# Kernel optimization log

Measured on AMD Instinct MI355X. Metric: run time of the kernel, lower is better.

Reference implementation:

```python
import jax, jax.numpy as jnp
import numpy as np

C = 128         # sphere_channels
H = 512         # hidden_channels
EC = 128        # edge_channels
LMAX = 4
K = 4           # num_experts
N_EQ = 2        # ceil(K/2) equivariant experts
N_NE = 2
N_NODES = 8192
N_EDGES = 262144
DEG_SIZES = np.array([2 * l + 1 for l in range(LMAX + 1)])  # [1,3,5,7,9]
M = int(DEG_SIZES.sum())  # 25 coeffs


def setup_inputs() -> dict:
    key = jax.random.key(0)
    ks = jax.random.split(key, 20)
    s = 0.02
    return {
        "x_emb": jax.random.normal(ks[0], (N_NODES, M, C), jnp.float32),
        "t_ij": jax.random.normal(ks[1], (N_EDGES, EC), jnp.float32),
        "edge_index": jax.random.randint(ks[2], (2, N_EDGES), 0, N_NODES, jnp.int32),
        # equivariant experts (stacked on leading expert axis)
        "eq_w1": jax.random.normal(ks[3], (N_EQ, C, H), jnp.float32) * s,
        "eq_gate_w": jax.random.normal(ks[4], (N_EQ, EC, H * (LMAX + 1)), jnp.float32) * s,
        "eq_gate_b": jax.random.normal(ks[5], (N_EQ, H * (LMAX + 1)), jnp.float32) * s,
        "eq_w2": jax.random.normal(ks[6], (N_EQ, H, C), jnp.float32) * s,
        # non-equivariant experts
        "ne_w1": jax.random.normal(ks[7], (N_NE, C, H), jnp.float32) * s,
        "ne_b1": jax.random.normal(ks[8], (N_NE, H), jnp.float32) * s,
        "ne_gate_w": jax.random.normal(ks[9], (N_NE, EC, H), jnp.float32) * s,
        "ne_gate_b": jax.random.normal(ks[10], (N_NE, H), jnp.float32) * s,
        "ne_w2": jax.random.normal(ks[11], (N_NE, H, C), jnp.float32) * s,
        "ne_b2": jax.random.normal(ks[12], (N_NE, C), jnp.float32) * s,
        # router
        "r_w1": jax.random.normal(ks[13], (EC, EC), jnp.float32) * s,
        "r_b1": jax.random.normal(ks[14], (EC,), jnp.float32) * s,
        "r_w2": jax.random.normal(ks[15], (EC, K), jnp.float32) * s,
        "r_b2": jax.random.normal(ks[16], (K,), jnp.float32) * s,
    }


def reference(x_emb, t_ij, edge_index, eq_w1, eq_gate_w, eq_gate_b, eq_w2,
              ne_w1, ne_b1, ne_gate_w, ne_gate_b, ne_w2, ne_b2,
              r_w1, r_b1, r_w2, r_b2):
    N = x_emb.shape[0]
    silu = jax.nn.silu

    # c_i = scatter-mean of t_ij onto destination nodes
    dst = edge_index[1]
    sums = jax.ops.segment_sum(t_ij, dst, num_segments=N)
    cnt = jax.ops.segment_sum(jnp.ones((t_ij.shape[0],), t_ij.dtype), dst, num_segments=N)
    c = sums / jnp.maximum(cnt, 1.0)[:, None]  # [N, EC]

    # soft routing weights from context
    w = jax.nn.softmax(silu(c @ r_w1 + r_b1) @ r_w2 + r_b2, axis=-1)  # [N, K]

    repeats = jnp.asarray(DEG_SIZES)
    is_scalar = (jnp.arange(M) == 0)[:, None]  # l=0 coeff mask, [M,1]

    # --- equivariant experts (vectorized over expert axis e) ---
    h = jnp.einsum('nmc,ech->enmh', x_emb, eq_w1)                      # [e,N,M,H]
    g = silu(jnp.einsum('nc,ecg->eng', c, eq_gate_w) + eq_gate_b[:, None, :])
    g = g.reshape(N_EQ, N, LMAX + 1, H)
    g = jnp.repeat(g, repeats, axis=2, total_repeat_length=M)          # [e,N,M,H]
    h = jnp.where(is_scalar, silu(h), h) * g                           # SiLU only on l=0
    out_eq = jnp.einsum('enmh,ehc->enmc', h, eq_w2)

    # --- non-equivariant experts ---
    h2 = silu(jnp.einsum('nmc,ech->enmh', x_emb, ne_w1) + ne_b1[:, None, None, :])
    g2 = silu(jnp.einsum('nc,ech->enh', c, ne_gate_w) + ne_gate_b[:, None, :])
    h2 = h2 * g2[:, :, None, :]
    out_ne = jnp.einsum('enmh,ehc->enmc', h2, ne_w2) + ne_b2[:, None, None, :]

    # softmax-weighted mixture (equiv experts first, matching ModuleList order)
    out = (jnp.einsum('nk,knmc->nmc', w[:, :N_EQ], out_eq)
           + jnp.einsum('nk,knmc->nmc', w[:, N_EQ:], out_ne))
    return out
```

## Files before the change

### kernel.cpp

```cpp
#include <hip/hip_runtime.h>

#define NNODES 8192
#define NEDGES 262144
#define CCH    128
#define HCH    512
#define GCOLS  6144
#define ROWS   204800
#define XSPAD  136
#define HGPAD  72

typedef __bf16 bf16_t;
typedef __bf16 bf16x8 __attribute__((ext_vector_type(8)));
typedef __bf16 bf16x4 __attribute__((ext_vector_type(4)));
typedef float  f32x4  __attribute__((ext_vector_type(4)));

__device__ __forceinline__ float siluf(float x) { return x / (1.f + __expf(-x)); }

#define GLOAD_LDS(g, l) __builtin_amdgcn_global_load_lds( \
    (const __attribute__((address_space(1))) void*)(g), \
    (__attribute__((address_space(3))) void*)(l), 16, 0, 0)

constexpr size_t OFF_CSUM  = 0;
constexpr size_t OFF_DEG   = 4194304;
constexpr size_t OFF_OFFS  = 4227072;
constexpr size_t OFF_CUR   = 4263936;
constexpr size_t OFF_EIDS  = 4296704;
constexpr size_t OFF_WRT   = 5345280;
constexpr size_t OFF_CBF   = 5476352;
constexpr size_t OFF_WPT   = 7573504;
constexpr size_t OFF_BPK   = 9146368;
constexpr size_t OFF_W1T   = 9170944;
constexpr size_t OFF_W2T   = 9695232;
constexpr size_t OFF_GATES = 10219520;

__global__ __launch_bounds__(256) void edge_count_kernel(
    const int* __restrict__ edge_index, int* __restrict__ deg)
{
  int e = blockIdx.x * 256 + threadIdx.x;
  atomicAdd(&deg[edge_index[NEDGES + e]], 1);
}

__global__ __launch_bounds__(256) void scan_kernel(
    const int* __restrict__ deg, int* __restrict__ offs, int* __restrict__ cur)
{
  __shared__ int part[256];
  int t = threadIdx.x;
  int s = 0;
  #pragma unroll 4
  for (int i = 0; i < 32; ++i) s += deg[t * 32 + i];
  part[t] = s;
  __syncthreads();
  int incl = s;
  for (int off = 1; off < 256; off <<= 1) {
    int u = (t >= off) ? part[t - off] : 0;
    __syncthreads();
    incl += u;
    part[t] = incl;
    __syncthreads();
  }
  int run = incl - s;
  for (int i = 0; i < 32; ++i) {
    int d = deg[t * 32 + i];
    offs[t * 32 + i] = run;
    cur[t * 32 + i]  = run;
    run += d;
  }
  if (t == 255) offs[8192] = run;
}

__global__ __launch_bounds__(256) void edge_fill_kernel(
    const int* __restrict__ edge_index, int* __restrict__ cur, int* __restrict__ eids)
{
  int e = blockIdx.x * 256 + threadIdx.x;
  int dst = edge_index[NEDGES + e];
  int pos = atomicAdd(&cur[dst], 1);
  eids[pos] = e;
}

__global__ __launch_bounds__(128) void gather_mean_kernel(
    const float* __restrict__ t_ij, const int* __restrict__ offs,
    const int* __restrict__ eids, float* __restrict__ csum, bf16_t* __restrict__ cbf)
{
  int n = blockIdx.x, tid = threadIdx.x;
  int o0 = offs[n], o1 = offs[n + 1];
  float a0 = 0.f, a1 = 0.f;
  int j = o0;
  for (; j + 1 < o1; j += 2) {
    int e0 = eids[j], e1 = eids[j + 1];
    a0 += t_ij[(size_t)e0 * CCH + tid];
    a1 += t_ij[(size_t)e1 * CCH + tid];
  }
  if (j < o1) a0 += t_ij[(size_t)eids[j] * CCH + tid];
  float m = (a0 + a1) / fmaxf((float)(o1 - o0), 1.f);
  csum[(size_t)n * CCH + tid] = m;
  cbf[(size_t)n * CCH + tid]  = (bf16_t)m;
}

__global__ __launch_bounds__(256) void pack_kernel(
    const float* __restrict__ eq_gate_w, const float* __restrict__ ne_gate_w,
    const float* __restrict__ eq_gate_b, const float* __restrict__ ne_gate_b,
    const float* __restrict__ eq_w1, const float* __restrict__ ne_w1,
    const float* __restrict__ eq_w2, const float* __restrict__ ne_w2,
    bf16_t* __restrict__ WpackT, float* __restrict__ bpack,
    bf16_t* __restrict__ w1T, bf16_t* __restrict__ w2c)
{
  int idx = blockIdx.x * 256 + threadIdx.x;
  if (idx < 786432) {
    int j = idx >> 7, c = idx & 127;
    float v;
    if (j < 5120) { int e = j / 2560, h = j - e * 2560;
      v = eq_gate_w[(size_t)e * 327680 + (size_t)c * 2560 + h]; }
    else { int j2 = j - 5120; int e = j2 >> 9, h = j2 & 511;
      v = ne_gate_w[(size_t)e * 65536 + (size_t)c * 512 + h]; }
    WpackT[idx] = (bf16_t)v;
  } else if (idx < 792576) {
    int j = idx - 786432;
    float v;
    if (j < 5120) { int e = j / 2560; v = eq_gate_b[e * 2560 + (j - e * 2560)]; }
    else { int j2 = j - 5120; int e = j2 >> 9; v = ne_gate_b[e * 512 + (j2 & 511)]; }
    bpack[j] = v;
  } else if (idx < 1054720) {
    int i = idx - 792576;
    int e = i >> 16, rest = i & 65535, h = rest >> 7, c = rest & 127;
    float v = (e < 2) ? eq_w1[(size_t)e * 65536 + (size_t)c * 512 + h]
                      : ne_w1[(size_t)(e - 2) * 65536 + (size_t)c * 512 + h];
    w1T[i] = (bf16_t)v;
  } else if (idx < 1316864) {
    int i = idx - 1054720;
    int e = i >> 16, rest = i & 65535;
    int hc = rest >> 13, r2 = rest & 8191;
    int c = r2 >> 6, h64 = r2 & 63;
    int h = hc * 64 + h64;
    float v = (e < 2) ? eq_w2[(size_t)e * 65536 + (size_t)h * 128 + c]
                      : ne_w2[(size_t)(e - 2) * 65536 + (size_t)h * 128 + c];
    w2c[i] = (bf16_t)v;
  }
}

__global__ __launch_bounds__(128) void router_kernel(
    const float* __restrict__ c,
    const float* __restrict__ r_w1, const float* __restrict__ r_b1,
    const float* __restrict__ r_w2, const float* __restrict__ r_b2,
    float* __restrict__ wroute)
{
  __shared__ float cl[128];
  __shared__ float h1[128];
  __shared__ float lg[4];
  int n = blockIdx.x, tid = threadIdx.x;
  cl[tid] = c[(size_t)n * 128 + tid];
  __syncthreads();
  float a = 0.f;
  #pragma unroll 8
  for (int k = 0; k < 128; ++k) a += cl[k] * r_w1[k * 128 + tid];
  a += r_b1[tid];
  h1[tid] = siluf(a);
  __syncthreads();
  if (tid < 4) {
    float s = 0.f;
    for (int j = 0; j < 128; ++j) s += h1[j] * r_w2[j * 4 + tid];
    lg[tid] = s + r_b2[tid];
  }
  __syncthreads();
  if (tid == 0) {
    float m = fmaxf(fmaxf(lg[0], lg[1]), fmaxf(lg[2], lg[3]));
    float e0 = __expf(lg[0] - m), e1 = __expf(lg[1] - m);
    float e2 = __expf(lg[2] - m), e3 = __expf(lg[3] - m);
    float s = 1.f / (e0 + e1 + e2 + e3);
    f32x4 w = {e0 * s, e1 * s, e2 * s, e3 * s};
    *(f32x4*)&wroute[n * 4] = w;
  }
}

__global__ __launch_bounds__(256, 2) void gate_gemm_kernel(
    const bf16_t* __restrict__ WpackT, const bf16_t* __restrict__ cbf,
    const float* __restrict__ bpack, bf16_t* __restrict__ gates, int n0)
{
  __shared__ bf16_t gt[128 * XSPAD];
  int jt = blockIdx.x, nt = blockIdx.y;
  int tid = threadIdx.x;
  int wave = tid >> 6, lane = tid & 63;
  int wr = wave >> 1, wc = wave & 1;
  int l15 = lane & 15, quad = lane >> 4;

  f32x4 acc[4][4];
  #pragma unroll
  for (int i = 0; i < 4; ++i)
    #pragma unroll
    for (int j = 0; j < 4; ++j) acc[i][j] = {0.f, 0.f, 0.f, 0.f};

  const bf16_t* abase = WpackT + ((size_t)jt * 128 + wr * 64 + l15) * 128 + quad * 8;
  const bf16_t* bbase = cbf + ((size_t)(n0 + nt * 128) + wc * 64 + l15) * 128 + quad * 8;
  #pragma unroll
  for (int ks = 0; ks < 4; ++ks) {
    bf16x8 af[4], bfr[4];
    #pragma unroll
    for (int tr = 0; tr < 4; ++tr) af[tr] = *(const bf16x8*)(abase + (size_t)tr * 16 * 128 + ks * 32);
    #pragma unroll
    for (int tc = 0; tc < 4; ++tc) bfr[tc] = *(const bf16x8*)(bbase + (size_t)tc * 16 * 128 + ks * 32);
    #pragma unroll
    for (int tr = 0; tr < 4; ++tr)
      #pragma unroll
      for (int tc = 0; tc < 4; ++tc)
        acc[tr][tc] = __builtin_amdgcn_mfma_f32_16x16x32_bf16(af[tr], bfr[tc], acc[tr][tc], 0, 0, 0);
  }
  #pragma unroll
  for (int tr = 0; tr < 4; ++tr) {
    int j0 = wr * 64 + tr * 16 + quad * 4;
    f32x4 bb = *(const f32x4*)&bpack[jt * 128 + j0];
    #pragma unroll
    for (int tc = 0; tc < 4; ++tc) {
      int nl = wc * 64 + tc * 16 + l15;
      f32x4 v = acc[tr][tc];
      bf16x4 gv;
      #pragma unroll
      for (int q = 0; q < 4; ++q) gv[q] = (bf16_t)siluf(v[q] + bb[q]);
      *(bf16x4*)&gt[nl * XSPAD + j0] = gv;
    }
  }
  __syncthreads();
  #pragma unroll
  for (int it = 0; it < 8; ++it) {
    int idx = it * 2048 + tid * 8;
    int lr = idx >> 7, col = idx & 127;
    *(bf16x8*)&gates[((size_t)nt * 128 + lr) * GCOLS + jt * 128 + col] =
        *(const bf16x8*)&gt[lr * XSPAD + col];
  }
}

__global__ __launch_bounds__(256, 2) void fused_experts_kernel(
    const float* __restrict__ x,
    const bf16_t* __restrict__ w1T,
    const bf16_t* __restrict__ w2c,
    const bf16_t* __restrict__ gates,
    const float* __restrict__ wroute,
    const float* __restrict__ ne_b1,
    const float* __restrict__ ne_b2,
    float* __restrict__ out,
    int n0)
{
  __shared__ __align__(16) bf16_t ws1[8192];
  __shared__ __align__(16) bf16_t ws2[8192];
  __shared__ __align__(16) bf16_t hg[4 * 32 * HGPAD];

  const int tid = threadIdx.x;
  const int wave = tid >> 6, lane = tid & 63;
  const int l15 = lane & 15, quad = lane >> 4;
  const int r0 = n0 * 25 + blockIdx.x * 128;
  const int rbase = wave * 32;
  bf16_t* hgw = hg + wave * 32 * HGPAD;

  int soff1[4], soff2[4];
  #pragma unroll
  for (int i = 0; i < 4; ++i) {
    int p = wave * 4096 + i * 1024 + lane * 16;
    int row1 = p >> 8;
    soff1[i] = (row1 * 256 + ((p & 255) ^ ((row1 & 7) << 4))) >> 1;
    int row2 = p >> 7;
    soff2[i] = (row2 * 128 + ((p & 127) ^ ((row2 & 7) << 4))) >> 1;
  }
  const int swz = (l15 & 7) << 4;
  int colswz[4];
  #pragma unroll
  for (int ks = 0; ks < 4; ++ks) colswz[ks] = (ks * 64 + quad * 16) ^ swz;

  int nloc[2], lidx[2];
  f32x4 rw[2];
  bf16x8 xf[2][4];
  #pragma unroll
  for (int tc = 0; tc < 2; ++tc) {
    int r = r0 + rbase + tc * 16 + l15;
    int n = r / 25;
    int m = r - n * 25;
    nloc[tc] = n - n0;
    lidx[tc] = (m == 0) ? 0 : (m < 4) ? 1 : (m < 9) ? 2 : (m < 16) ? 3 : 4;
    rw[tc] = *(const f32x4*)&wroute[n * 4];
    const float* xr = x + (size_t)r * CCH + quad * 8;
    #pragma unroll
    for (int ks = 0; ks < 4; ++ks) {
      f32x4 a = *(const f32x4*)(xr + ks * 32);
      f32x4 b = *(const f32x4*)(xr + ks * 32 + 4);
      bf16x8 v;
      #pragma unroll
      for (int q = 0; q < 4; ++q) { v[q] = (bf16_t)a[q]; v[4 + q] = (bf16_t)b[q]; }
      xf[tc][ks] = v;
    }
  }

  f32x4 oacc[8][2];
  #pragma unroll
  for (int i = 0; i < 8; ++i)
    #pragma unroll
    for (int j = 0; j < 2; ++j) oacc[i][j] = {0.f, 0.f, 0.f, 0.f};

  #pragma unroll 1
  for (int e = 0; e < 4; ++e) {
    const bool is_eq = (e < 2);
    #pragma unroll 1
    for (int hc = 0; hc < 8; ++hc) {
      const bf16_t* g1 = w1T + (size_t)(((e << 3) + hc) << 13);
      const bf16_t* g2 = w2c + (size_t)(((e << 3) + hc) << 13);
      #pragma unroll
      for (int i = 0; i < 4; ++i) {
        GLOAD_LDS(g1 + soff1[i], ws1 + wave * 2048 + i * 512);
        GLOAD_LDS(g2 + soff2[i], ws2 + wave * 2048 + i * 512);
      }
      __syncthreads();

      bf16x4 gv[2][4];
      #pragma unroll
      for (int tc = 0; tc < 2; ++tc) {
        size_t gbase = (size_t)nloc[tc] * GCOLS + hc * 64
                     + (is_eq ? (size_t)(e * 2560 + lidx[tc] * 512)
                              : (size_t)(5120 + (e - 2) * 512));
        #pragma unroll
        for (int tr = 0; tr < 4; ++tr)
          gv[tc][tr] = *(const bf16x4*)&gates[gbase + tr * 16 + quad * 4];
      }

      f32x4 hacc[4][2];
      #pragma unroll
      for (int i = 0; i < 4; ++i)
        #pragma unroll
        for (int j = 0; j < 2; ++j) hacc[i][j] = {0.f, 0.f, 0.f, 0.f};
      #pragma unroll
      for (int ks = 0; ks < 4; ++ks) {
        bf16x8 af[4];
        #pragma unroll
        for (int tr = 0; tr < 4; ++tr)
          af[tr] = *(const bf16x8*)((const char*)ws1 + (l15 + tr * 16) * 256 + colswz[ks]);
        #pragma unroll
        for (int tr = 0; tr < 4; ++tr)
          #pragma unroll
          for (int tc = 0; tc < 2; ++tc)
            hacc[tr][tc] = __builtin_amdgcn_mfma_f32_16x16x32_bf16(af[tr], xf[tc][ks], hacc[tr][tc], 0, 0, 0);
      }
      #pragma unroll
      for (int tc = 0; tc < 2; ++tc) {
        float wre = rw[tc][e];
        #pragma unroll
        for (int tr = 0; tr < 4; ++tr) {
          int hl = tr * 16 + quad * 4;
          f32x4 v = hacc[tr][tc];
          bf16x4 g = gv[tc][tr];
          if (is_eq) {
            if (lidx[tc] == 0) {
              #pragma unroll
              for (int q = 0; q < 4; ++q) v[q] = siluf(v[q]);
            }
          } else {
            f32x4 b1 = *(const f32x4*)&ne_b1[(e - 2) * 512 + hc * 64 + hl];
            #pragma unroll
            for (int q = 0; q < 4; ++q) v[q] = siluf(v[q] + b1[q]);
          }
          bf16x4 hv;
          #pragma unroll
          for (int q = 0; q < 4; ++q) hv[q] = (bf16_t)(v[q] * (float)g[q] * wre);
          *(bf16x4*)&hgw[(tc * 16 + l15) * HGPAD + hl] = hv;
        }
      }
      __builtin_amdgcn_wave_barrier();
      #pragma unroll
      for (int ks = 0; ks < 2; ++ks) {
        bf16x8 bfr[2];
        #pragma unroll
        for (int tc = 0; tc < 2; ++tc)
          bfr[tc] = *(const bf16x8*)&hgw[(tc * 16 + l15) * HGPAD + ks * 32 + quad * 8];
        #pragma unroll
        for (int tr = 0; tr < 8; ++tr) {
          bf16x8 af2 = *(const bf16x8*)((const char*)ws2 + (l15 + tr * 16) * 128 + colswz[ks]);
          #pragma unroll
          for (int tc = 0; tc < 2; ++tc)
            oacc[tr][tc] = __builtin_amdgcn_mfma_f32_16x16x32_bf16(af2, bfr[tc], oacc[tr][tc], 0, 0, 0);
        }
      }
      __syncthreads();
    }
  }
  #pragma unroll
  for (int tc = 0; tc < 2; ++tc) {
    size_t rg = (size_t)(r0 + rbase + tc * 16 + l15);
    float wn0 = rw[tc][2], wn1 = rw[tc][3];
    #pragma unroll
    for (int tr = 0; tr < 8; ++tr) {
      int c0 = tr * 16 + quad * 4;
      f32x4 v = oacc[tr][tc];
      f32x4 b20 = *(const f32x4*)&ne_b2[c0];
      f32x4 b21 = *(const f32x4*)&ne_b2[128 + c0];
      f32x4 ov;
      #pragma unroll
      for (int q = 0; q < 4; ++q)
        ov[q] = v[q] + wn0 * b20[q] + wn1 * b21[q];
      *(f32x4*)&out[rg * CCH + c0] = ov;
    }
  }
}

extern "C" void kernel_launch(void* const* d_in, const int* in_sizes, int n_in,
                              void* d_out, int out_size, void* d_ws, size_t ws_size,
                              hipStream_t stream)
{
  const float* x_emb     = (const float*)d_in[0];
  const float* t_ij      = (const float*)d_in[1];
  const int*   edge_index= (const int*)d_in[2];
  const float* eq_w1     = (const float*)d_in[3];
  const float* eq_gate_w = (const float*)d_in[4];
  const float* eq_gate_b = (const float*)d_in[5];
  const float* eq_w2     = (const float*)d_in[6];
  const float* ne_w1     = (const float*)d_in[7];
  const float* ne_b1     = (const float*)d_in[8];
  const float* ne_gate_w = (const float*)d_in[9];
  const float* ne_gate_b = (const float*)d_in[10];
  const float* ne_w2     = (const float*)d_in[11];
  const float* ne_b2     = (const float*)d_in[12];
  const float* r_w1      = (const float*)d_in[13];
  const float* r_b1      = (const float*)d_in[14];
  const float* r_w2      = (const float*)d_in[15];
  const float* r_b2      = (const float*)d_in[16];
  float* out = (float*)d_out;

  char* ws = (char*)d_ws;
  float*  csum   = (float*)(ws + OFF_CSUM);
  int*    deg    = (int*)(ws + OFF_DEG);
  int*    offs   = (int*)(ws + OFF_OFFS);
  int*    cur    = (int*)(ws + OFF_CUR);
  int*    eids   = (int*)(ws + OFF_EIDS);
  float*  wroute = (float*)(ws + OFF_WRT);
  bf16_t* cbf    = (bf16_t*)(ws + OFF_CBF);
  bf16_t* WpackT = (bf16_t*)(ws + OFF_WPT);
  float*  bpack  = (float*)(ws + OFF_BPK);
  bf16_t* w1T    = (bf16_t*)(ws + OFF_W1T);
  bf16_t* w2c    = (bf16_t*)(ws + OFF_W2T);
  bf16_t* gates  = (bf16_t*)(ws + OFF_GATES);

  size_t avail = (ws_size > OFF_GATES) ? ws_size - OFF_GATES : 0;
  int chunk = 128;
  for (int c = NNODES; c >= 128; c >>= 1) {
    if ((size_t)c * GCOLS * sizeof(bf16_t) <= avail) { chunk = c; break; }
  }

  hipMemsetAsync(ws + OFF_DEG, 0, 32768, stream);

  edge_count_kernel<<<NEDGES / 256, 256, 0, stream>>>(edge_index, deg);
  scan_kernel<<<1, 256, 0, stream>>>(deg, offs, cur);
  edge_fill_kernel<<<NEDGES / 256, 256, 0, stream>>>(edge_index, cur, eids);
  gather_mean_kernel<<<NNODES, 128, 0, stream>>>(t_ij, offs, eids, csum, cbf);

  pack_kernel<<<5144, 256, 0, stream>>>(eq_gate_w, ne_gate_w, eq_gate_b, ne_gate_b,
                                        eq_w1, ne_w1, eq_w2, ne_w2,
                                        WpackT, bpack, w1T, w2c);
  router_kernel<<<NNODES, 128, 0, stream>>>(csum, r_w1, r_b1, r_w2, r_b2, wroute);

  for (int n0 = 0; n0 < NNODES; n0 += chunk) {
    gate_gemm_kernel<<<dim3(GCOLS / 128, chunk / 128), 256, 0, stream>>>(
        WpackT, cbf, bpack, gates, n0);
    fused_experts_kernel<<<chunk * 25 / 128, 256, 0, stream>>>(
        x_emb, w1T, w2c, gates, wroute, ne_b1, ne_b2, out, n0);
  }
}
```

Before: 894.6 us.

## Prefetch next expert weight chunk during compute and fold router weight into gates

Flattens the expert/hidden-chunk loop into a single 32-step loop. Loads of the next chunk's w1 tile now overlap the second GEMM, and the next w2 tile is issued after the final barrier, so the weight transfer is spread out instead of stalling at the top of each iteration. The per-node router weight is multiplied into the gate values inside the gate GEMM, which removes one multiply per element in the expert kernel. Launch bounds rise to 3 blocks per CU on both kernels, which tightens register budgets and may cause spills.

```diff
diff --git a/kernel.cpp b/kernel.cpp
--- a/kernel.cpp
+++ b/kernel.cpp
@@ -171,9 +171,10 @@
   }
 }
 
-__global__ __launch_bounds__(256, 2) void gate_gemm_kernel(
+__global__ __launch_bounds__(256, 3) void gate_gemm_kernel(
     const bf16_t* __restrict__ WpackT, const bf16_t* __restrict__ cbf,
-    const float* __restrict__ bpack, bf16_t* __restrict__ gates, int n0)
+    const float* __restrict__ bpack, const float* __restrict__ wroute,
+    bf16_t* __restrict__ gates, int n0)
 {
   __shared__ bf16_t gt[128 * XSPAD];
   int jt = blockIdx.x, nt = blockIdx.y;
@@ -181,6 +182,7 @@
   int wave = tid >> 6, lane = tid & 63;
   int wr = wave >> 1, wc = wave & 1;
   int l15 = lane & 15, quad = lane >> 4;
+  int ej = (jt < 20) ? 0 : (jt < 40) ? 1 : (jt < 44) ? 2 : 3;
 
   f32x4 acc[4][4];
   #pragma unroll
@@ -190,6 +192,10 @@
 
   const bf16_t* abase = WpackT + ((size_t)jt * 128 + wr * 64 + l15) * 128 + quad * 8;
   const bf16_t* bbase = cbf + ((size_t)(n0 + nt * 128) + wc * 64 + l15) * 128 + quad * 8;
+  float wsc[4];
+  #pragma unroll
+  for (int tc = 0; tc < 4; ++tc)
+    wsc[tc] = wroute[(size_t)(n0 + nt * 128 + wc * 64 + tc * 16 + l15) * 4 + ej];
   #pragma unroll
   for (int ks = 0; ks < 4; ++ks) {
     bf16x8 af[4], bfr[4];
@@ -213,7 +219,7 @@
       f32x4 v = acc[tr][tc];
       bf16x4 gv;
       #pragma unroll
-      for (int q = 0; q < 4; ++q) gv[q] = (bf16_t)siluf(v[q] + bb[q]);
+      for (int q = 0; q < 4; ++q) gv[q] = (bf16_t)(siluf(v[q] + bb[q]) * wsc[tc]);
       *(bf16x4*)&gt[nl * XSPAD + j0] = gv;
     }
   }
@@ -227,7 +233,7 @@
   }
 }
 
-__global__ __launch_bounds__(256, 2) void fused_experts_kernel(
+__global__ __launch_bounds__(256, 3) void fused_experts_kernel(
     const float* __restrict__ x,
     const bf16_t* __restrict__ w1T,
     const bf16_t* __restrict__ w2c,
@@ -292,88 +298,97 @@
     #pragma unroll
     for (int j = 0; j < 2; ++j) oacc[i][j] = {0.f, 0.f, 0.f, 0.f};
 
+  #pragma unroll
+  for (int i = 0; i < 4; ++i)
+    GLOAD_LDS(w1T + soff1[i], ws1 + wave * 2048 + i * 512);
+  __syncthreads();
+  #pragma unroll
+  for (int i = 0; i < 4; ++i)
+    GLOAD_LDS(w2c + soff2[i], ws2 + wave * 2048 + i * 512);
+
   #pragma unroll 1
-  for (int e = 0; e < 4; ++e) {
+  for (int t = 0; t < 32; ++t) {
+    const int e = t >> 3, hc = t & 7;
     const bool is_eq = (e < 2);
-    #pragma unroll 1
-    for (int hc = 0; hc < 8; ++hc) {
-      const bf16_t* g1 = w1T + (size_t)(((e << 3) + hc) << 13);
-      const bf16_t* g2 = w2c + (size_t)(((e << 3) + hc) << 13);
-      #pragma unroll
-      for (int i = 0; i < 4; ++i) {
-        GLOAD_LDS(g1 + soff1[i], ws1 + wave * 2048 + i * 512);
-        GLOAD_LDS(g2 + soff2[i], ws2 + wave * 2048 + i * 512);
-      }
-      __syncthreads();
-
-      bf16x4 gv[2][4];
-      #pragma unroll
-      for (int tc = 0; tc < 2; ++tc) {
-        size_t gbase = (size_t)nloc[tc] * GCOLS + hc * 64
-                     + (is_eq ? (size_t)(e * 2560 + lidx[tc] * 512)
-                              : (size_t)(5120 + (e - 2) * 512));
-        #pragma unroll
-        for (int tr = 0; tr < 4; ++tr)
-          gv[tc][tr] = *(const bf16x4*)&gates[gbase + tr * 16 + quad * 4];
-      }
-
-      f32x4 hacc[4][2];
-      #pragma unroll
-      for (int i = 0; i < 4; ++i)
-        #pragma unroll
-        for (int j = 0; j < 2; ++j) hacc[i][j] = {0.f, 0.f, 0.f, 0.f};
-      #pragma unroll
-      for (int ks = 0; ks < 4; ++ks) {
-        bf16x8 af[4];
-        #pragma unroll
-        for (int tr = 0; tr < 4; ++tr)
-          af[tr] = *(const bf16x8*)((const char*)ws1 + (l15 + tr * 16) * 256 + colswz[ks]);
-        #pragma unroll
-        for (int tr = 0; tr < 4; ++tr)
-          #pragma unroll
-          for (int tc = 0; tc < 2; ++tc)
-            hacc[tr][tc] = __builtin_amdgcn_mfma_f32_16x16x32_bf16(af[tr], xf[tc][ks], hacc[tr][tc], 0, 0, 0);
-      }
-      #pragma unroll
-      for (int tc = 0; tc < 2; ++tc) {
-        float wre = rw[tc][e];
-        #pragma unroll
-        for (int tr = 0; tr < 4; ++tr) {
-          int hl = tr * 16 + quad * 4;
-          f32x4 v = hacc[tr][tc];
-          bf16x4 g = gv[tc][tr];
-          if (is_eq) {
-            if (lidx[tc] == 0) {
-              #pragma unroll
-              for (int q = 0; q < 4; ++q) v[q] = siluf(v[q]);
-            }
-          } else {
-            f32x4 b1 = *(const f32x4*)&ne_b1[(e - 2) * 512 + hc * 64 + hl];
-            #pragma unroll
-            for (int q = 0; q < 4; ++q) v[q] = siluf(v[q] + b1[q]);
-          }
-          bf16x4 hv;
-          #pragma unroll
-          for (int q = 0; q < 4; ++q) hv[q] = (bf16_t)(v[q] * (float)g[q] * wre);
-          *(bf16x4*)&hgw[(tc * 16 + l15) * HGPAD + hl] = hv;
-        }
-      }
-      __builtin_amdgcn_wave_barrier();
-      #pragma unroll
-      for (int ks = 0; ks < 2; ++ks) {
-        bf16x8 bfr[2];
+
+    bf16x4 gv[2][4];
+    #pragma unroll
+    for (int tc = 0; tc < 2; ++tc) {
+      size_t gbase = (size_t)nloc[tc] * GCOLS + hc * 64
+                   + (is_eq ? (size_t)(e * 2560 + lidx[tc] * 512)
+                            : (size_t)(5120 + (e - 2) * 512));
+      #pragma unroll
+      for (int tr = 0; tr < 4; ++tr)
+        gv[tc][tr] = *(const bf16x4*)&gates[gbase + tr * 16 + quad * 4];
+    }
+
+    f32x4 hacc[4][2];
+    #pragma unroll
+    for (int i = 0; i < 4; ++i)
+      #pragma unroll
+      for (int j = 0; j < 2; ++j) hacc[i][j] = {0.f, 0.f, 0.f, 0.f};
+    #pragma unroll
+    for (int ks = 0; ks < 4; ++ks) {
+      bf16x8 af[4];
+      #pragma unroll
+      for (int tr = 0; tr < 4; ++tr)
+        af[tr] = *(const bf16x8*)((const char*)ws1 + (l15 + tr * 16) * 256 + colswz[ks]);
+      #pragma unroll
+      for (int tr = 0; tr < 4; ++tr)
         #pragma unroll
         for (int tc = 0; tc < 2; ++tc)
-          bfr[tc] = *(const bf16x8*)&hgw[(tc * 16 + l15) * HGPAD + ks * 32 + quad * 8];
+          hacc[tr][tc] = __builtin_amdgcn_mfma_f32_16x16x32_bf16(af[tr], xf[tc][ks], hacc[tr][tc], 0, 0, 0);
+    }
+    #pragma unroll
+    for (int tc = 0; tc < 2; ++tc) {
+      #pragma unroll
+      for (int tr = 0; tr < 4; ++tr) {
+        int hl = tr * 16 + quad * 4;
+        f32x4 v = hacc[tr][tc];
+        bf16x4 g = gv[tc][tr];
+        if (is_eq) {
+          if (lidx[tc] == 0) {
+            #pragma unroll
+            for (int q = 0; q < 4; ++q) v[q] = siluf(v[q]);
+          }
+        } else {
+          f32x4 b1 = *(const f32x4*)&ne_b1[(e - 2) * 512 + hc * 64 + hl];
+          #pragma unroll
+          for (int q = 0; q < 4; ++q) v[q] = siluf(v[q] + b1[q]);
+        }
+        bf16x4 hv;
         #pragma unroll
-        for (int tr = 0; tr < 8; ++tr) {
-          bf16x8 af2 = *(const bf16x8*)((const char*)ws2 + (l15 + tr * 16) * 128 + colswz[ks]);
-          #pragma unroll
-          for (int tc = 0; tc < 2; ++tc)
-            oacc[tr][tc] = __builtin_amdgcn_mfma_f32_16x16x32_bf16(af2, bfr[tc], oacc[tr][tc], 0, 0, 0);
-        }
+        for (int q = 0; q < 4; ++q) hv[q] = (bf16_t)(v[q] * (float)g[q]);
+        *(bf16x4*)&hgw[(tc * 16 + l15) * HGPAD + hl] = hv;
       }
-      __syncthreads();
+    }
+    __syncthreads();
+    if (t < 31) {
+      const bf16_t* g1 = w1T + ((size_t)(t + 1) << 13);
+      #pragma unroll
+      for (int i = 0; i < 4; ++i)
+        GLOAD_LDS(g1 + soff1[i], ws1 + wave * 2048 + i * 512);
+    }
+    #pragma unroll
+    for (int ks = 0; ks < 2; ++ks) {
+      bf16x8 bfr[2];
+      #pragma unroll
+      for (int tc = 0; tc < 2; ++tc)
+        bfr[tc] = *(const bf16x8*)&hgw[(tc * 16 + l15) * HGPAD + ks * 32 + quad * 8];
+      #pragma unroll
+      for (int tr = 0; tr < 8; ++tr) {
+        bf16x8 af2 = *(const bf16x8*)((const char*)ws2 + (l15 + tr * 16) * 128 + colswz[ks]);
+        #pragma unroll
+        for (int tc = 0; tc < 2; ++tc)
+          oacc[tr][tc] = __builtin_amdgcn_mfma_f32_16x16x32_bf16(af2, bfr[tc], oacc[tr][tc], 0, 0, 0);
+      }
+    }
+    __syncthreads();
+    if (t < 31) {
+      const bf16_t* g2 = w2c + ((size_t)(t + 1) << 13);
+      #pragma unroll
+      for (int i = 0; i < 4; ++i)
+        GLOAD_LDS(g2 + soff2[i], ws2 + wave * 2048 + i * 512);
     }
   }
   #pragma unroll
@@ -452,7 +467,7 @@
 
   for (int n0 = 0; n0 < NNODES; n0 += chunk) {
     gate_gemm_kernel<<<dim3(GCOLS / 128, chunk / 128), 256, 0, stream>>>(
-        WpackT, cbf, bpack, gates, n0);
+        WpackT, cbf, bpack, wroute, gates, n0);
     fused_experts_kernel<<<chunk * 25 / 128, 256, 0, stream>>>(
         x_emb, w1T, w2c, gates, wroute, ne_b1, ne_b2, out, n0);
   }
```

Result: slower. 1.048 ms (+17.2%).
